# Kernel tuning notes

Hardware: AMD Instinct MI355X
Metric: run time of the kernel (lower is better)

## Reference

```python
import jax, jax.numpy as jnp
import numpy as np
from jax import lax

NPG = 61      # nodes (electrodes) per graph, hard-coded by 61*hidden reshape
B = 128       # graphs per batch
L = 160       # raw signal length -> final conv length 1
NF = 64       # num_features
HC = 128      # hidden_channels
NCLS = 4


def setup_inputs() -> dict:
    key = jax.random.key(0)
    ks = jax.random.split(key, 16)
    N = B * NPG
    # fully-connected (no self-loops) edges within each graph -> 3660 edges/graph
    a = np.repeat(np.arange(NPG), NPG)
    b = np.tile(np.arange(NPG), NPG)
    m = a != b
    sl, dl = a[m], b[m]
    off = (np.arange(B) * NPG)[:, None]
    edge_index = np.stack([(sl[None] + off).ravel(), (dl[None] + off).ravel()]).astype(np.int64)
    batch = np.repeat(np.arange(B), NPG).astype(np.int64)

    def rn(k, shape, fan_in):
        return jax.random.normal(k, shape, jnp.float32) / np.sqrt(fan_in).astype(np.float32)

    return dict(
        x=jax.random.normal(ks[0], (N, L), jnp.float32),
        edge_index=jnp.asarray(edge_index),
        batch=jnp.asarray(batch),
        edge_features=jax.random.normal(ks[1], (edge_index.shape[1], 3), jnp.float32),
        conv_w0=rn(ks[2], (NF, 1, 7), 7.0), conv_b0=jnp.zeros((NF,), jnp.float32),
        conv_w1=rn(ks[3], (NF, NF, 5), NF * 5.0), conv_b1=jnp.zeros((NF,), jnp.float32),
        conv_w2=rn(ks[4], (NF, NF, 3), NF * 3.0), conv_b2=jnp.zeros((NF,), jnp.float32),
        bn1_g=jnp.ones((NF,), jnp.float32), bn1_b=jnp.zeros((NF,), jnp.float32),
        g_w0=rn(ks[5], (NF, HC), float(NF)), g_b0=jnp.zeros((HC,), jnp.float32),
        g_w1=rn(ks[6], (HC, HC), float(HC)), g_b1=jnp.zeros((HC,), jnp.float32),
        g_w2=rn(ks[7], (HC, HC), float(HC)), g_b2=jnp.zeros((HC,), jnp.float32),
        bn2_g=jnp.ones((HC,), jnp.float32), bn2_b=jnp.zeros((HC,), jnp.float32),
        lin_w0=rn(ks[8], (NPG * HC, HC), float(NPG * HC)), lin_b0=jnp.zeros((HC,), jnp.float32),
        lin_w1=rn(ks[9], (HC, HC), float(HC)), lin_b1=jnp.zeros((HC,), jnp.float32),
        lin_w2=rn(ks[10], (HC, NCLS), float(HC)), lin_b2=jnp.zeros((NCLS,), jnp.float32),
        edge_w=rn(ks[11], (3, 1), 3.0), edge_b=jnp.zeros((1,), jnp.float32),
    )


def _conv1d(x, w, b, pad):
    # x: [N, Cin, L], w: [Cout, Cin, K]
    y = lax.conv_general_dilated(x, w, (1,), [(pad, pad)], dimension_numbers=('NCH', 'OIH', 'NCH'))
    return y + b[None, :, None]


def _maxpool7(x):
    n = x.shape[-1] // 7
    return x[..., : n * 7].reshape(x.shape[0], x.shape[1], n, 7).max(-1)


def _bn(x, g, b):
    # BatchNorm1d in training mode: biased batch statistics
    m = x.mean(0)
    v = x.var(0)
    return (x - m) * lax.rsqrt(v + 1e-5) * g + b


def _forward(x, edge_features, conv_w0, conv_b0, conv_w1, conv_b1, conv_w2, conv_b2,
             bn1_g, bn1_b, g_w0, g_b0, g_w1, g_b1, g_w2, g_b2, bn2_g, bn2_b,
             lin_w0, lin_b0, lin_w1, lin_b1, lin_w2, lin_b2, edge_w, edge_b,
             edge_index, batch):
    N = x.shape[0]
    nb = N // NPG  # == batch.max()+1 for contiguous graph layout
    # tanh-gated edge weights
    ew = jnp.tanh(edge_features @ edge_w + edge_b)            # [E, 1]
    # Conv1d feature extractor: [N,1,160] -> [N,NF,1]
    h = x[:, None, :]
    h = _maxpool7(jax.nn.relu(_conv1d(h, conv_w0, conv_b0, 0)))   # [N,NF,22]
    h = jax.nn.relu(_conv1d(h, conv_w1, conv_b1, 2))               # [N,NF,22]
    h = _maxpool7(h)                                               # [N,NF,3]
    h = _conv1d(h, conv_w2, conv_b2, 0)[:, :, 0]                   # [N,NF]
    h = _bn(h, bn1_g, bn1_b)
    # Edge-weighted GCN hops (MyzConv): lin -> gather src -> scale -> scatter-add dst
    src, dst = edge_index[0], edge_index[1]
    for w, bs, act in ((g_w0, g_b0, True), (g_w1, g_b1, True), (g_w2, g_b2, False)):
        hw = h @ w + bs                                            # [N,HC]
        msg = ew * hw[src]                                         # [E,HC]
        h = jax.ops.segment_sum(msg, dst, num_segments=N)
        if act:
            h = jax.nn.relu(h)
    h = _bn(h, bn2_g, bn2_b)
    # MLP classifier over concatenated node features per graph
    h = h.reshape(nb, NPG * HC)
    h = jax.nn.relu(h @ lin_w0 + lin_b0)
    h = jax.nn.relu(h @ lin_w1 + lin_b1)
    h = h @ lin_w2 + lin_b2
    return jax.nn.log_softmax(h, -1), ew.reshape(nb, -1).T


def reference(x, edge_index, batch, edge_features, conv_w0, conv_b0, conv_w1, conv_b1,
              conv_w2, conv_b2, bn1_g, bn1_b, g_w0, g_b0, g_w1, g_b1, g_w2, g_b2,
              bn2_g, bn2_b, lin_w0, lin_b0, lin_w1, lin_b1, lin_w2, lin_b2, edge_w, edge_b):
    return _forward(x, edge_features, conv_w0, conv_b0, conv_w1, conv_b1, conv_w2, conv_b2,
                    bn1_g, bn1_b, g_w0, g_b0, g_w1, g_b1, g_w2, g_b2, bn2_g, bn2_b,
                    lin_w0, lin_b0, lin_w1, lin_b1, lin_w2, lin_b2, edge_w, edge_b,
                    edge_index, batch)
```

## Files before the change

kernel.cpp:

```cpp
#include <hip/hip_runtime.h>
#include <math.h>

#define NPGN 61
#define NGRAPH 128
#define NNODES (NPGN*NGRAPH)
#define EPG 3660
#define NCONVB (NNODES/4)

typedef float float4v __attribute__((ext_vector_type(4)));
typedef short bf16x8 __attribute__((ext_vector_type(8)));
typedef unsigned short u16;

__device__ __forceinline__ u16 f2bf(float v){
  union { float f; unsigned u; } x; x.f = v;
  unsigned r = (x.u + 0x7FFFu + ((x.u >> 16) & 1u)) >> 16;
  return (u16)r;
}
__device__ __forceinline__ float bf2f(unsigned u){
  union { unsigned u; float f; } x; x.u = u << 16;
  return x.f;
}

__global__ __launch_bounds__(256) void k_prep(const float* __restrict__ w0,
    const float* __restrict__ w1, const float* __restrict__ w2,
    const float* __restrict__ gw0, const float* __restrict__ gw1, const float* __restrict__ gw2,
    const float* __restrict__ lw0,
    float* __restrict__ w0t, u16* __restrict__ w1b, u16* __restrict__ w2b,
    u16* __restrict__ gwt0, u16* __restrict__ gwt1, u16* __restrict__ gwt2,
    u16* __restrict__ lw0t, float* __restrict__ accs){
  __shared__ __align__(16) u16 tile[32*132];
  int b = blockIdx.x, tid = threadIdx.x;
  if (b >= 534){
    int idx = (b - 534)*256 + tid;
    if (idx < 20480) accs[idx] = 0.f;
    return;
  }
  if (b < 290){
    int idx = b*256 + tid;
    if (idx < 20480){
      int f = idx / 320, r = idx - f*320;
      int kk = r >> 6, c = r & 63;
      w1b[idx] = f2bf(w1[f*320 + c*5 + kk]);
    } else if (idx < 32768){
      int j = idx - 20480; w2b[j] = f2bf(w2[j]);
    } else if (idx < 40960){
      int j = idx - 32768; int jj = j >> 6, k = j & 63; gwt0[j] = f2bf(gw0[k*128 + jj]);
    } else if (idx < 57344){
      int j = idx - 40960; int jj = j >> 7, k = j & 127; gwt1[j] = f2bf(gw1[k*128 + jj]);
    } else if (idx < 73728){
      int j = idx - 57344; int jj = j >> 7, k = j & 127; gwt2[j] = f2bf(gw2[k*128 + jj]);
    } else if (idx < 74176){
      int j = idx - 73728; int k = j >> 6, f = j & 63; w0t[j] = w0[f*7 + k];
    }
  } else {
    int bb = b - 290;
    int i = bb >> 2, oq = bb & 3;
    for (int idx = tid; idx < 4096; idx += 256){
      int k = idx >> 5, ol = idx & 31;
      tile[ol*132 + k] = f2bf(lw0[((size_t)i*128 + k)*128 + oq*32 + ol]);
    }
    __syncthreads();
    unsigned* dst = (unsigned*)lw0t;
    for (int idx = tid; idx < 2048; idx += 256){
      int ol = idx >> 6, kw = idx & 63;
      unsigned v = (unsigned)tile[ol*132 + 2*kw] | ((unsigned)tile[ol*132 + 2*kw + 1] << 16);
      dst[((size_t)i*128 + oq*32 + ol)*64 + kw] = v;
    }
  }
}

#define A0T_STR 72
#define A0T_ROWS 28
#define C1_STR 24
#define NB 4
#define EW_STR 72
__global__ __launch_bounds__(256) void k_conv(const float* __restrict__ x,
    const float* __restrict__ w0t, const float* __restrict__ b0,
    const u16* __restrict__ w1b, const float* __restrict__ b1,
    const u16* __restrict__ w2b, const float* __restrict__ b2,
    float* __restrict__ h0, float* __restrict__ stat1p,
    const float* __restrict__ ef, const float* __restrict__ eww,
    const float* __restrict__ ewb, float* __restrict__ out2,
    u16* __restrict__ ews){
  int tid = threadIdx.x;
  if (blockIdx.x < NGRAPH){
    int g = blockIdx.x;
    u16* eg = ews + (size_t)g*(64*EW_STR);
    for (int idx = tid; idx < 64*EW_STR; idx += 256) eg[idx] = 0;
    __syncthreads();
    float v0 = eww[0], v1 = eww[1], v2 = eww[2], bb = ewb[0];
    const float* efg = ef + (size_t)g*EPG*3;
    for (int idx = tid; idx < EPG; idx += 256){
      const float* p = efg + idx*3;
      float v = tanhf(p[0]*v0 + p[1]*v1 + p[2]*v2 + bb);
      int s = idx/60, r = idx - s*60;
      int d = r + (r >= s ? 1 : 0);
      eg[d*EW_STR + s] = f2bf(v);
      out2[(size_t)idx*128 + g] = v;
    }
    return;
  }
  int cb = blockIdx.x - NGRAPH;

  int w = tid >> 6, lane = tid & 63;
  int q = lane >> 4, r16 = lane & 15;
  __shared__ __align__(16) float xs[NB][160];
  __shared__ __align__(16) u16 a0t[NB][A0T_ROWS*A0T_STR];
  __shared__ __align__(16) u16 c1s[NB][64*C1_STR];
  __shared__ __align__(16) u16 a1k[NB][208];

  {
    const float* xb = x + (size_t)cb*NB*160;
    float* xsf = &xs[0][0];
    #pragma unroll
    for (int idx = tid; idx < NB*160; idx += 256) xsf[idx] = xb[idx];
  }

  bf16x8 wf1[10], wf2[6];
  #pragma unroll
  for (int ks = 0; ks < 10; ks++)
    wf1[ks] = *(const bf16x8*)(w1b + (16*w + r16)*320 + ks*32 + q*8);
  #pragma unroll
  for (int ks = 0; ks < 6; ks++)
    wf2[ks] = *(const bf16x8*)(w2b + (16*w + r16)*192 + ks*32 + q*8);
  float4 b1v = *(const float4*)(b1 + 16*w + 4*q);
  float4 b2v = *(const float4*)(b2 + 16*w + 4*q);

  float w0r[7];
  #pragma unroll
  for (int k = 0; k < 7; k++) w0r[k] = w0t[k*64 + lane];
  float b0f = b0[lane];

  #pragma unroll
  for (int i2 = 0; i2 < 6; i2++){
    int rp = (i2 < 2) ? i2 : 22 + i2;
    a0t[w][rp*A0T_STR + lane] = 0;
  }
  __syncthreads();

  for (int j = w; j < 44; j += 4){
    int n = j / 11, qp = j - n*11;
    const float* xsp = &xs[n][0];
    float win[20];
    #pragma unroll
    for (int jj = 0; jj < 20; jj++) win[jj] = xsp[14*qp + jj];
    float m0, m1;
    #pragma unroll
    for (int r = 0; r < 7; r++){
      float s = w0r[0]*win[r];
      #pragma unroll
      for (int k = 1; k < 7; k++) s += w0r[k]*win[r+k];
      m0 = r ? fmaxf(m0, s) : s;
    }
    #pragma unroll
    for (int r = 7; r < 14; r++){
      float s = w0r[0]*win[r];
      #pragma unroll
      for (int k = 1; k < 7; k++) s += w0r[k]*win[r+k];
      m1 = (r > 7) ? fmaxf(m1, s) : s;
    }
    a0t[n][(2 + 2*qp)*A0T_STR + lane] = f2bf(fmaxf(m0 + b0f, 0.f));
    a0t[n][(3 + 2*qp)*A0T_STR + lane] = f2bf(fmaxf(m1 + b0f, 0.f));
  }
  __syncthreads();

  #pragma unroll 1
  for (int n = 0; n < NB; n++){
    float4v acc0 = {0.f,0.f,0.f,0.f}, acc1 = {0.f,0.f,0.f,0.f};
    #pragma unroll
    for (int ks = 0; ks < 10; ks++){
      int kk = ks >> 1;
      int cbase = (ks & 1)*32 + q*8;
      bf16x8 bv0 = *(const bf16x8*)(&a0t[n][(r16 + kk)*A0T_STR + cbase]);
      bf16x8 bv1 = *(const bf16x8*)(&a0t[n][(r16 + 16 + kk)*A0T_STR + cbase]);
      acc0 = __builtin_amdgcn_mfma_f32_16x16x32_bf16(wf1[ks], bv0, acc0, 0, 0, 0);
      acc1 = __builtin_amdgcn_mfma_f32_16x16x32_bf16(wf1[ks], bv1, acc1, 0, 0, 0);
    }
    #pragma unroll
    for (int reg = 0; reg < 4; reg++){
      int m = 16*w + q*4 + reg;
      float bv_ = ((const float*)&b1v)[reg];
      c1s[n][m*C1_STR + r16] = f2bf(fmaxf(acc0[reg] + bv_, 0.f));
      if (r16 <= 4)
        c1s[n][m*C1_STR + 16 + r16] = f2bf(fmaxf(acc1[reg] + bv_, 0.f));
    }
  }
  __syncthreads();

  {
    const u16* c1 = &c1s[w][0];
    bf16x8 f0 = *(const bf16x8*)(c1 + lane*C1_STR);
    bf16x8 f1 = *(const bf16x8*)(c1 + lane*C1_STR + 8);
    bf16x8 f2 = *(const bf16x8*)(c1 + lane*C1_STR + 16);
    float v[24];
    #pragma unroll
    for (int j = 0; j < 8; j++){
      v[j]    = bf2f((u16)f0[j]);
      v[8+j]  = bf2f((u16)f1[j]);
      v[16+j] = bf2f((u16)f2[j]);
    }
    #pragma unroll
    for (int t = 0; t < 3; t++){
      float m = v[t*7];
      #pragma unroll
      for (int r = 1; r < 7; r++) m = fmaxf(m, v[t*7+r]);
      a1k[w][lane*3 + t] = f2bf(m);
    }
  }
  __syncthreads();

  float4v sacc = {0.f,0.f,0.f,0.f}, qacc = {0.f,0.f,0.f,0.f};
  #pragma unroll 1
  for (int n = 0; n < NB; n++){
    float4v acc2 = {0.f,0.f,0.f,0.f};
    #pragma unroll
    for (int ks = 0; ks < 6; ks++){
      bf16x8 bs = *(const bf16x8*)(&a1k[n][ks*32 + q*8]);
      acc2 = __builtin_amdgcn_mfma_f32_16x16x32_bf16(wf2[ks], bs, acc2, 0, 0, 0);
    }
    if (r16 == 0){
      int nn = cb*NB + n;
      #pragma unroll
      for (int reg = 0; reg < 4; reg++){
        int f = 16*w + 4*q + reg;
        float v = acc2[reg] + ((const float*)&b2v)[reg];
        h0[(size_t)nn*64 + f] = v;
        sacc[reg] += v;
        qacc[reg] += v*v;
      }
    }
  }

  if (r16 == 0){
    int bkt = cb & 31;
    #pragma unroll
    for (int reg = 0; reg < 4; reg++){
      int f = 16*w + 4*q + reg;
      atomicAdd(&stat1p[bkt*128 + f], sacc[reg]);
      atomicAdd(&stat1p[bkt*128 + 64 + f], qacc[reg]);
    }
  }
}

#define HS_STR 136
#define HWT_STR 72
__global__ __launch_bounds__(512) void k_gnn(const float* __restrict__ h0,
    const float* __restrict__ stat1p,
    const float* __restrict__ bn1g, const float* __restrict__ bn1b,
    const u16* __restrict__ gwt0, const float* __restrict__ gb0,
    const u16* __restrict__ gwt1, const float* __restrict__ gb1,
    const u16* __restrict__ gwt2, const float* __restrict__ gb2,
    const u16* __restrict__ ews,
    u16* __restrict__ hB, float* __restrict__ stat2p){
  int g = blockIdx.x, tid = threadIdx.x;
  int w = tid >> 6, lane = tid & 63, q = lane >> 4, r16 = lane & 15;
  int dt = w & 3, jh = w >> 2;
  __shared__ u16 hs[64*HS_STR];
  __shared__ u16 hwT[128*HWT_STR];
  __shared__ float bsc[64], bsh[64];
  __shared__ float st2[256];

  bf16x8 af0[2], af1[4], af2[4], ewf[2];
  #pragma unroll
  for (int ks = 0; ks < 2; ks++)
    af0[ks] = *(const bf16x8*)(gwt0 + (16*w + r16)*64 + ks*32 + q*8);
  #pragma unroll
  for (int ks = 0; ks < 4; ks++)
    af1[ks] = *(const bf16x8*)(gwt1 + (16*w + r16)*128 + ks*32 + q*8);
  #pragma unroll
  for (int ks = 0; ks < 4; ks++)
    af2[ks] = *(const bf16x8*)(gwt2 + (16*w + r16)*128 + ks*32 + q*8);
  #pragma unroll
  for (int ks = 0; ks < 2; ks++)
    ewf[ks] = *(const bf16x8*)(ews + (size_t)g*(64*EW_STR) + (16*dt + r16)*EW_STR + ks*32 + q*8);
  float4 b40 = *(const float4*)(gb0 + 16*w + 4*q);
  float4 b41 = *(const float4*)(gb1 + 16*w + 4*q);
  float4 b42 = *(const float4*)(gb2 + 16*w + 4*q);

  if (tid < 64){
    float s = 0.f, s2 = 0.f;
    #pragma unroll
    for (int r = 0; r < 32; r++){
      s  += stat1p[r*128 + tid];
      s2 += stat1p[r*128 + 64 + tid];
    }
    float m = s*(1.f/NNODES), v = s2*(1.f/NNODES) - m*m;
    float sc = rsqrtf(v + 1e-5f)*bn1g[tid];
    bsc[tid] = sc; bsh[tid] = bn1b[tid] - m*sc;
  }
  if (tid < 256) st2[tid] = 0.f;
  {
    unsigned* hsd = (unsigned*)hs;
    for (int idx = tid; idx < 3*(HS_STR/2); idx += 512){
      int rr = 61 + idx/(HS_STR/2), cc = idx%(HS_STR/2);
      hsd[rr*(HS_STR/2) + cc] = 0;
    }
  }
  __syncthreads();

  {
    unsigned* hsd = (unsigned*)hs;
    for (int idx = tid; idx < 61*32; idx += 512){
      int i = idx >> 5, kw = idx & 31;
      float2 hv = *(const float2*)(h0 + ((size_t)g*61 + i)*64 + kw*2);
      int k0 = kw*2;
      float a = hv.x*bsc[k0] + bsh[k0];
      float b = hv.y*bsc[k0+1] + bsh[k0+1];
      hsd[i*(HS_STR/2) + kw] = (unsigned)f2bf(a) | ((unsigned)f2bf(b) << 16);
    }
  }
  __syncthreads();

  #pragma unroll
  for (int nt = 0; nt < 4; nt++){
    float4v acc = {b40.x, b40.y, b40.z, b40.w};
    #pragma unroll
    for (int ks = 0; ks < 2; ks++){
      bf16x8 bv = *(const bf16x8*)(hs + (nt*16 + r16)*HS_STR + ks*32 + q*8);
      acc = __builtin_amdgcn_mfma_f32_16x16x32_bf16(af0[ks], bv, acc, 0, 0, 0);
    }
    #pragma unroll
    for (int r = 0; r < 4; r++)
      hwT[(16*w + 4*q + r)*HWT_STR + nt*16 + r16] = f2bf(acc[r]);
  }
  __syncthreads();
  #pragma unroll
  for (int nt = 0; nt < 4; nt++){
    int j = (jh*4 + nt)*16;
    float4v acc = {0.f,0.f,0.f,0.f};
    #pragma unroll
    for (int ks = 0; ks < 2; ks++){
      bf16x8 bv = *(const bf16x8*)(hwT + (j + r16)*HWT_STR + ks*32 + q*8);
      acc = __builtin_amdgcn_mfma_f32_16x16x32_bf16(ewf[ks], bv, acc, 0, 0, 0);
    }
    #pragma unroll
    for (int r = 0; r < 4; r++){
      int d = 16*dt + 4*q + r;
      hs[d*HS_STR + j + r16] = f2bf(fmaxf(acc[r], 0.f));
    }
  }
  __syncthreads();

  #pragma unroll
  for (int nt = 0; nt < 4; nt++){
    float4v acc = {b41.x, b41.y, b41.z, b41.w};
    #pragma unroll
    for (int ks = 0; ks < 4; ks++){
      bf16x8 bv = *(const bf16x8*)(hs + (nt*16 + r16)*HS_STR + ks*32 + q*8);
      acc = __builtin_amdgcn_mfma_f32_16x16x32_bf16(af1[ks], bv, acc, 0, 0, 0);
    }
    #pragma unroll
    for (int r = 0; r < 4; r++)
      hwT[(16*w + 4*q + r)*HWT_STR + nt*16 + r16] = f2bf(acc[r]);
  }
  __syncthreads();
  #pragma unroll
  for (int nt = 0; nt < 4; nt++){
    int j = (jh*4 + nt)*16;
    float4v acc = {0.f,0.f,0.f,0.f};
    #pragma unroll
    for (int ks = 0; ks < 2; ks++){
      bf16x8 bv = *(const bf16x8*)(hwT + (j + r16)*HWT_STR + ks*32 + q*8);
      acc = __builtin_amdgcn_mfma_f32_16x16x32_bf16(ewf[ks], bv, acc, 0, 0, 0);
    }
    #pragma unroll
    for (int r = 0; r < 4; r++){
      int d = 16*dt + 4*q + r;
      hs[d*HS_STR + j + r16] = f2bf(fmaxf(acc[r], 0.f));
    }
  }
  __syncthreads();

  #pragma unroll
  for (int nt = 0; nt < 4; nt++){
    float4v acc = {b42.x, b42.y, b42.z, b42.w};
    #pragma unroll
    for (int ks = 0; ks < 4; ks++){
      bf16x8 bv = *(const bf16x8*)(hs + (nt*16 + r16)*HS_STR + ks*32 + q*8);
      acc = __builtin_amdgcn_mfma_f32_16x16x32_bf16(af2[ks], bv, acc, 0, 0, 0);
    }
    #pragma unroll
    for (int r = 0; r < 4; r++)
      hwT[(16*w + 4*q + r)*HWT_STR + nt*16 + r16] = f2bf(acc[r]);
  }
  __syncthreads();
  #pragma unroll
  for (int nt = 0; nt < 4; nt++){
    int j = (jh*4 + nt)*16;
    float4v acc = {0.f,0.f,0.f,0.f};
    #pragma unroll
    for (int ks = 0; ks < 2; ks++){
      bf16x8 bv = *(const bf16x8*)(hwT + (j + r16)*HWT_STR + ks*32 + q*8);
      acc = __builtin_amdgcn_mfma_f32_16x16x32_bf16(ewf[ks], bv, acc, 0, 0, 0);
    }
    float cs = 0.f, cq = 0.f;
    #pragma unroll
    for (int r = 0; r < 4; r++){
      int d = 16*dt + 4*q + r;
      if (d < 61){
        float v = acc[r];
        hB[((size_t)g*61 + d)*128 + j + r16] = f2bf(v);
        cs += v; cq += v*v;
      }
    }
    int col = j + r16;
    atomicAdd(&st2[col], cs);
    atomicAdd(&st2[128 + col], cq);
  }
  __syncthreads();
  if (tid < 256) stat2p[(size_t)tid*128 + g] = st2[tid];
}

#define AS_STR 136
__global__ __launch_bounds__(256) void k_mlp0(const u16* __restrict__ hB,
    const float* __restrict__ stat2p,
    const float* __restrict__ bn2g, const float* __restrict__ bn2b,
    const u16* __restrict__ lw0t, float* __restrict__ y0pre){
  int bi = blockIdx.x; int i = bi >> 2, sub = bi & 3;
  int oh = sub & 1, gh = sub >> 1;
  int tid = threadIdx.x, w = tid >> 6, lane = tid & 63, q = lane >> 4, r16 = lane & 15;
  __shared__ u16 As[64*AS_STR];
  __shared__ float sc2[128], sh2[128];
  if (tid < 128){
    float4v sa = {0,0,0,0}, sb = {0,0,0,0};
    #pragma unroll
    for (int r = 0; r < 32; r++){
      sa += *(const float4v*)(stat2p + (size_t)tid*128 + r*4);
      sb += *(const float4v*)(stat2p + (size_t)(128 + tid)*128 + r*4);
    }
    float s = sa[0]+sa[1]+sa[2]+sa[3], s2 = sb[0]+sb[1]+sb[2]+sb[3];
    float m = s*(1.f/NNODES), v = s2*(1.f/NNODES) - m*m;
    float sc = rsqrtf(v + 1e-5f)*bn2g[tid];
    sc2[tid] = sc; sh2[tid] = bn2b[tid] - m*sc;
  }
  __syncthreads();
  {
    const unsigned* hbd = (const unsigned*)hB;
    unsigned* asd = (unsigned*)As;
    for (int idx = tid; idx < 4096; idx += 256){
      int gg = gh*64 + (idx >> 6), kw = idx & 63;
      unsigned pv = hbd[((size_t)gg*61 + i)*64 + kw];
      int k0 = kw*2;
      float a = bf2f(pv & 0xffffu)*sc2[k0] + sh2[k0];
      float b = bf2f(pv >> 16)*sc2[k0+1] + sh2[k0+1];
      asd[(idx >> 6)*(AS_STR/2) + kw] = (unsigned)f2bf(a) | ((unsigned)f2bf(b) << 16);
    }
  }
  __syncthreads();
  const u16* wbase = lw0t + ((size_t)i*128 + oh*64)*128;
  bf16x8 af[4];
  #pragma unroll
  for (int ks = 0; ks < 4; ks++)
    af[ks] = *(const bf16x8*)(As + (16*w + r16)*AS_STR + ks*32 + q*8);
  #pragma unroll
  for (int nt = 0; nt < 4; nt++){
    float4v acc = {0.f,0.f,0.f,0.f};
    #pragma unroll
    for (int ks = 0; ks < 4; ks++){
      bf16x8 bv = *(const bf16x8*)(wbase + (size_t)(nt*16 + r16)*128 + ks*32 + q*8);
      acc = __builtin_amdgcn_mfma_f32_16x16x32_bf16(af[ks], bv, acc, 0, 0, 0);
    }
    #pragma unroll
    for (int r = 0; r < 4; r++){
      int g = gh*64 + 16*w + 4*q + r;
      atomicAdd(&y0pre[(size_t)g*128 + oh*64 + nt*16 + r16], acc[r]);
    }
  }
}

__global__ __launch_bounds__(128) void k_mlp1(const float* __restrict__ y0pre,
    const float* __restrict__ lb0, const float* __restrict__ W1,
    const float* __restrict__ lb1, const float* __restrict__ W2,
    const float* __restrict__ lb2, float* __restrict__ out){
  int g = blockIdx.x, o = threadIdx.x;
  __shared__ float y0[128], y1[128], red[128];
  y0[o] = fmaxf(y0pre[(size_t)g*128 + o] + lb0[o], 0.f);
  __syncthreads();
  float a = lb1[o];
  #pragma unroll 8
  for (int k = 0; k < 128; k++) a += y0[k]*W1[k*128 + o];
  y1[o] = fmaxf(a, 0.f);
  __syncthreads();
  int c = o & 3, kb = o >> 2;
  float a2 = 0.f;
  #pragma unroll
  for (int j = 0; j < 4; j++){
    int k = kb + 32*j;
    a2 += y1[k]*W2[k*4 + c];
  }
  red[o] = a2;
  __syncthreads();
  #pragma unroll
  for (int off = 64; off >= 4; off >>= 1){
    if (o < off) red[o] += red[o + off];
    __syncthreads();
  }
  if (o == 0){
    float v0 = red[0]+lb2[0], v1 = red[1]+lb2[1], v2 = red[2]+lb2[2], v3 = red[3]+lb2[3];
    float m = fmaxf(fmaxf(v0,v1), fmaxf(v2,v3));
    float lse = m + logf(expf(v0-m)+expf(v1-m)+expf(v2-m)+expf(v3-m));
    out[g*4+0]=v0-lse; out[g*4+1]=v1-lse; out[g*4+2]=v2-lse; out[g*4+3]=v3-lse;
  }
}

extern "C" void kernel_launch(void* const* d_in, const int* in_sizes, int n_in,
                              void* d_out, int out_size, void* d_ws, size_t ws_size,
                              hipStream_t stream){
  const float* x    = (const float*)d_in[0];
  const float* ef   = (const float*)d_in[3];
  const float* cw0  = (const float*)d_in[4];
  const float* cb0  = (const float*)d_in[5];
  const float* cw1  = (const float*)d_in[6];
  const float* cb1  = (const float*)d_in[7];
  const float* cw2  = (const float*)d_in[8];
  const float* cb2  = (const float*)d_in[9];
  const float* bn1g = (const float*)d_in[10];
  const float* bn1b = (const float*)d_in[11];
  const float* gw0  = (const float*)d_in[12];
  const float* gb0  = (const float*)d_in[13];
  const float* gw1  = (const float*)d_in[14];
  const float* gb1  = (const float*)d_in[15];
  const float* gw2  = (const float*)d_in[16];
  const float* gb2  = (const float*)d_in[17];
  const float* bn2g = (const float*)d_in[18];
  const float* bn2b = (const float*)d_in[19];
  const float* lw0  = (const float*)d_in[20];
  const float* lb0  = (const float*)d_in[21];
  const float* lw1  = (const float*)d_in[22];
  const float* lb1  = (const float*)d_in[23];
  const float* lw2  = (const float*)d_in[24];
  const float* lb2  = (const float*)d_in[25];
  const float* eww  = (const float*)d_in[26];
  const float* ewb  = (const float*)d_in[27];
  float* out = (float*)d_out;

  float* ws   = (float*)d_ws;
  float* w1s  = ws;
  float* w2s  = w1s + 10240;
  float* w0t  = w2s + 6144;
  float* gws0 = w0t + 448;
  float* gws1 = gws0 + 4096;
  float* gws2 = gws1 + 8192;
  float* h0   = gws2 + 8192;
  float* hBs  = h0 + 499712;
  float* lw0s = hBs + 499712;
  float* accs = lw0s + 499712;
  float* ewss = accs + 53248;

  u16* w1b    = (u16*)w1s;
  u16* w2b    = (u16*)w2s;
  u16* gwt0   = (u16*)gws0;
  u16* gwt1   = (u16*)gws1;
  u16* gwt2   = (u16*)gws2;
  u16* hB     = (u16*)hBs;
  u16* lw0t   = (u16*)lw0s;
  u16* ews    = (u16*)ewss;
  float* stat1p = accs;
  float* y0pre  = accs + 4096;
  float* stat2p = accs + 20480;

  k_prep <<<615, 256, 0, stream>>>(cw0, cw1, cw2, gw0, gw1, gw2, lw0,
                                   w0t, w1b, w2b, gwt0, gwt1, gwt2, lw0t, accs);
  k_conv <<<NCONVB + NGRAPH, 256, 0, stream>>>(x, w0t, cb0, w1b, cb1, w2b, cb2,
                                               h0, stat1p, ef, eww, ewb,
                                               out + 512, ews);
  k_gnn  <<<NGRAPH, 512, 0, stream>>>(h0, stat1p, bn1g, bn1b,
                                      gwt0, gb0, gwt1, gb1, gwt2, gb2,
                                      ews, hB, stat2p);
  k_mlp0 <<<NPGN*4, 256, 0, stream>>>(hB, stat2p, bn2g, bn2b, lw0t, y0pre);
  k_mlp1 <<<NGRAPH, 128, 0, stream>>>(y0pre, lb0, lw1, lb1, lw2, lb2, out);
}
```

Before: 195.7 us.

## Drop weight-prep kernel and convert fp32 weights to bf16 inside consumer kernels

Removes the separate k_prep kernel that transposed and converted conv, GNN and MLP weights to bf16 in workspace. Each consumer kernel now reads the original fp32 weights with strided scalar loads and converts them in registers, and the accumulator zeroing becomes a hipMemsetAsync. This saves one launch plus the write and re-read of converted weights. In exchange the weight loads are uncoalesced gathers, repeated across many blocks, most notably the large lin_w0 reads in k_mlp0.

```diff
diff --git a/kernel.cpp b/kernel.cpp
--- a/kernel.cpp
+++ b/kernel.cpp
@@ -19,54 +19,6 @@
 __device__ __forceinline__ float bf2f(unsigned u){
   union { unsigned u; float f; } x; x.u = u << 16;
   return x.f;
-}
-
-__global__ __launch_bounds__(256) void k_prep(const float* __restrict__ w0,
-    const float* __restrict__ w1, const float* __restrict__ w2,
-    const float* __restrict__ gw0, const float* __restrict__ gw1, const float* __restrict__ gw2,
-    const float* __restrict__ lw0,
-    float* __restrict__ w0t, u16* __restrict__ w1b, u16* __restrict__ w2b,
-    u16* __restrict__ gwt0, u16* __restrict__ gwt1, u16* __restrict__ gwt2,
-    u16* __restrict__ lw0t, float* __restrict__ accs){
-  __shared__ __align__(16) u16 tile[32*132];
-  int b = blockIdx.x, tid = threadIdx.x;
-  if (b >= 534){
-    int idx = (b - 534)*256 + tid;
-    if (idx < 20480) accs[idx] = 0.f;
-    return;
-  }
-  if (b < 290){
-    int idx = b*256 + tid;
-    if (idx < 20480){
-      int f = idx / 320, r = idx - f*320;
-      int kk = r >> 6, c = r & 63;
-      w1b[idx] = f2bf(w1[f*320 + c*5 + kk]);
-    } else if (idx < 32768){
-      int j = idx - 20480; w2b[j] = f2bf(w2[j]);
-    } else if (idx < 40960){
-      int j = idx - 32768; int jj = j >> 6, k = j & 63; gwt0[j] = f2bf(gw0[k*128 + jj]);
-    } else if (idx < 57344){
-      int j = idx - 40960; int jj = j >> 7, k = j & 127; gwt1[j] = f2bf(gw1[k*128 + jj]);
-    } else if (idx < 73728){
-      int j = idx - 57344; int jj = j >> 7, k = j & 127; gwt2[j] = f2bf(gw2[k*128 + jj]);
-    } else if (idx < 74176){
-      int j = idx - 73728; int k = j >> 6, f = j & 63; w0t[j] = w0[f*7 + k];
-    }
-  } else {
-    int bb = b - 290;
-    int i = bb >> 2, oq = bb & 3;
-    for (int idx = tid; idx < 4096; idx += 256){
-      int k = idx >> 5, ol = idx & 31;
-      tile[ol*132 + k] = f2bf(lw0[((size_t)i*128 + k)*128 + oq*32 + ol]);
-    }
-    __syncthreads();
-    unsigned* dst = (unsigned*)lw0t;
-    for (int idx = tid; idx < 2048; idx += 256){
-      int ol = idx >> 6, kw = idx & 63;
-      unsigned v = (unsigned)tile[ol*132 + 2*kw] | ((unsigned)tile[ol*132 + 2*kw + 1] << 16);
-      dst[((size_t)i*128 + oq*32 + ol)*64 + kw] = v;
-    }
-  }
 }
 
 #define A0T_STR 72
@@ -75,9 +27,9 @@
 #define NB 4
 #define EW_STR 72
 __global__ __launch_bounds__(256) void k_conv(const float* __restrict__ x,
-    const float* __restrict__ w0t, const float* __restrict__ b0,
-    const u16* __restrict__ w1b, const float* __restrict__ b1,
-    const u16* __restrict__ w2b, const float* __restrict__ b2,
+    const float* __restrict__ cw0, const float* __restrict__ b0,
+    const float* __restrict__ cw1, const float* __restrict__ b1,
+    const float* __restrict__ cw2, const float* __restrict__ b2,
     float* __restrict__ h0, float* __restrict__ stat1p,
     const float* __restrict__ ef, const float* __restrict__ eww,
     const float* __restrict__ ewb, float* __restrict__ out2,
@@ -116,19 +68,31 @@
     for (int idx = tid; idx < NB*160; idx += 256) xsf[idx] = xb[idx];
   }
 
+  int f0_ = 16*w + r16;
   bf16x8 wf1[10], wf2[6];
   #pragma unroll
-  for (int ks = 0; ks < 10; ks++)
-    wf1[ks] = *(const bf16x8*)(w1b + (16*w + r16)*320 + ks*32 + q*8);
-  #pragma unroll
-  for (int ks = 0; ks < 6; ks++)
-    wf2[ks] = *(const bf16x8*)(w2b + (16*w + r16)*192 + ks*32 + q*8);
+  for (int ks = 0; ks < 10; ks++){
+    int kk = ks >> 1, cbse = (ks & 1)*32 + q*8;
+    const float* src = cw1 + (size_t)f0_*320 + kk;
+    bf16x8 v;
+    #pragma unroll
+    for (int j = 0; j < 8; j++) v[j] = (short)f2bf(src[(cbse + j)*5]);
+    wf1[ks] = v;
+  }
+  #pragma unroll
+  for (int ks = 0; ks < 6; ks++){
+    const float* src = cw2 + (size_t)f0_*192 + ks*32 + q*8;
+    bf16x8 v;
+    #pragma unroll
+    for (int j = 0; j < 8; j++) v[j] = (short)f2bf(src[j]);
+    wf2[ks] = v;
+  }
   float4 b1v = *(const float4*)(b1 + 16*w + 4*q);
   float4 b2v = *(const float4*)(b2 + 16*w + 4*q);
 
   float w0r[7];
   #pragma unroll
-  for (int k = 0; k < 7; k++) w0r[k] = w0t[k*64 + lane];
+  for (int k = 0; k < 7; k++) w0r[k] = cw0[lane*7 + k];
   float b0f = b0[lane];
 
   #pragma unroll
@@ -247,9 +211,9 @@
 __global__ __launch_bounds__(512) void k_gnn(const float* __restrict__ h0,
     const float* __restrict__ stat1p,
     const float* __restrict__ bn1g, const float* __restrict__ bn1b,
-    const u16* __restrict__ gwt0, const float* __restrict__ gb0,
-    const u16* __restrict__ gwt1, const float* __restrict__ gb1,
-    const u16* __restrict__ gwt2, const float* __restrict__ gb2,
+    const float* __restrict__ gw0, const float* __restrict__ gb0,
+    const float* __restrict__ gw1, const float* __restrict__ gb1,
+    const float* __restrict__ gw2, const float* __restrict__ gb2,
     const u16* __restrict__ ews,
     u16* __restrict__ hB, float* __restrict__ stat2p){
   int g = blockIdx.x, tid = threadIdx.x;
@@ -260,16 +224,29 @@
   __shared__ float bsc[64], bsh[64];
   __shared__ float st2[256];
 
+  int jj_ = 16*w + r16;
   bf16x8 af0[2], af1[4], af2[4], ewf[2];
   #pragma unroll
-  for (int ks = 0; ks < 2; ks++)
-    af0[ks] = *(const bf16x8*)(gwt0 + (16*w + r16)*64 + ks*32 + q*8);
-  #pragma unroll
-  for (int ks = 0; ks < 4; ks++)
-    af1[ks] = *(const bf16x8*)(gwt1 + (16*w + r16)*128 + ks*32 + q*8);
-  #pragma unroll
-  for (int ks = 0; ks < 4; ks++)
-    af2[ks] = *(const bf16x8*)(gwt2 + (16*w + r16)*128 + ks*32 + q*8);
+  for (int ks = 0; ks < 2; ks++){
+    bf16x8 v;
+    #pragma unroll
+    for (int j = 0; j < 8; j++) v[j] = (short)f2bf(gw0[(size_t)(ks*32 + q*8 + j)*128 + jj_]);
+    af0[ks] = v;
+  }
+  #pragma unroll
+  for (int ks = 0; ks < 4; ks++){
+    bf16x8 v;
+    #pragma unroll
+    for (int j = 0; j < 8; j++) v[j] = (short)f2bf(gw1[(size_t)(ks*32 + q*8 + j)*128 + jj_]);
+    af1[ks] = v;
+  }
+  #pragma unroll
+  for (int ks = 0; ks < 4; ks++){
+    bf16x8 v;
+    #pragma unroll
+    for (int j = 0; j < 8; j++) v[j] = (short)f2bf(gw2[(size_t)(ks*32 + q*8 + j)*128 + jj_]);
+    af2[ks] = v;
+  }
   #pragma unroll
   for (int ks = 0; ks < 2; ks++)
     ewf[ks] = *(const bf16x8*)(ews + (size_t)g*(64*EW_STR) + (16*dt + r16)*EW_STR + ks*32 + q*8);
@@ -415,7 +392,7 @@
 __global__ __launch_bounds__(256) void k_mlp0(const u16* __restrict__ hB,
     const float* __restrict__ stat2p,
     const float* __restrict__ bn2g, const float* __restrict__ bn2b,
-    const u16* __restrict__ lw0t, float* __restrict__ y0pre){
+    const float* __restrict__ lw0, float* __restrict__ y0pre){
   int bi = blockIdx.x; int i = bi >> 2, sub = bi & 3;
   int oh = sub & 1, gh = sub >> 1;
   int tid = threadIdx.x, w = tid >> 6, lane = tid & 63, q = lane >> 4, r16 = lane & 15;
@@ -447,17 +424,20 @@
     }
   }
   __syncthreads();
-  const u16* wbase = lw0t + ((size_t)i*128 + oh*64)*128;
   bf16x8 af[4];
   #pragma unroll
   for (int ks = 0; ks < 4; ks++)
     af[ks] = *(const bf16x8*)(As + (16*w + r16)*AS_STR + ks*32 + q*8);
   #pragma unroll
   for (int nt = 0; nt < 4; nt++){
+    int o_ = oh*64 + nt*16 + r16;
     float4v acc = {0.f,0.f,0.f,0.f};
     #pragma unroll
     for (int ks = 0; ks < 4; ks++){
-      bf16x8 bv = *(const bf16x8*)(wbase + (size_t)(nt*16 + r16)*128 + ks*32 + q*8);
+      bf16x8 bv;
+      #pragma unroll
+      for (int j = 0; j < 8; j++)
+        bv[j] = (short)f2bf(lw0[((size_t)i*128 + ks*32 + q*8 + j)*128 + o_]);
       acc = __builtin_amdgcn_mfma_f32_16x16x32_bf16(af[ks], bv, acc, 0, 0, 0);
     }
     #pragma unroll
@@ -535,38 +515,24 @@
   float* out = (float*)d_out;
 
   float* ws   = (float*)d_ws;
-  float* w1s  = ws;
-  float* w2s  = w1s + 10240;
-  float* w0t  = w2s + 6144;
-  float* gws0 = w0t + 448;
-  float* gws1 = gws0 + 4096;
-  float* gws2 = gws1 + 8192;
-  float* h0   = gws2 + 8192;
+  float* h0   = ws;
   float* hBs  = h0 + 499712;
-  float* lw0s = hBs + 499712;
-  float* accs = lw0s + 499712;
+  float* accs = hBs + 499712;
   float* ewss = accs + 53248;
 
-  u16* w1b    = (u16*)w1s;
-  u16* w2b    = (u16*)w2s;
-  u16* gwt0   = (u16*)gws0;
-  u16* gwt1   = (u16*)gws1;
-  u16* gwt2   = (u16*)gws2;
   u16* hB     = (u16*)hBs;
-  u16* lw0t   = (u16*)lw0s;
   u16* ews    = (u16*)ewss;
   float* stat1p = accs;
   float* y0pre  = accs + 4096;
   float* stat2p = accs + 20480;
 
-  k_prep <<<615, 256, 0, stream>>>(cw0, cw1, cw2, gw0, gw1, gw2, lw0,
-                                   w0t, w1b, w2b, gwt0, gwt1, gwt2, lw0t, accs);
-  k_conv <<<NCONVB + NGRAPH, 256, 0, stream>>>(x, w0t, cb0, w1b, cb1, w2b, cb2,
+  hipMemsetAsync(accs, 0, 20480*sizeof(float), stream);
+  k_conv <<<NCONVB + NGRAPH, 256, 0, stream>>>(x, cw0, cb0, cw1, cb1, cw2, cb2,
                                                h0, stat1p, ef, eww, ewb,
                                                out + 512, ews);
   k_gnn  <<<NGRAPH, 512, 0, stream>>>(h0, stat1p, bn1g, bn1b,
-                                      gwt0, gb0, gwt1, gb1, gwt2, gb2,
+                                      gw0, gb0, gw1, gb1, gw2, gb2,
                                       ews, hB, stat2p);
-  k_mlp0 <<<NPGN*4, 256, 0, stream>>>(hB, stat2p, bn2g, bn2b, lw0t, y0pre);
+  k_mlp0 <<<NPGN*4, 256, 0, stream>>>(hB, stat2p, bn2g, bn2b, lw0, y0pre);
   k_mlp1 <<<NGRAPH, 128, 0, stream>>>(y0pre, lb0, lw1, lb1, lw2, lb2, out);
 }
```

Result: slower. 213.5 us (+9.1%).
